# Performance work log

Measured on AMD Instinct MI355X. Metric: run time of the kernel, lower is better.

Reference implementation:

```python
import jax, jax.numpy as jnp
import numpy as np
from jax import lax

# --- static config (mirrors cfg / init args) ---
B, T, F_IN = 4, 1024, 80      # batch, time steps, mel bins (80 -> freq collapses to 1)
C_EMB = 512                   # cfg.dim_embed
C0 = C_EMB // 2               # first_conv_filters (non-tcn branch)
HEADS, K = 8, 7               # num_heads, NA kernel_size (dilation=1)
D_HEAD = C_EMB // HEADS
MLP = 4 * C_EMB               # mlp_ratio=4
EPS = 1e-5                    # layer_norm_eps


def setup_inputs() -> dict:
    key = jax.random.key(0)
    ks = jax.random.split(key, 16)
    rn = lambda k, s, sc=0.02: jax.random.normal(k, s, dtype=jnp.float32) * sc
    z = lambda *s: jnp.zeros(s, dtype=jnp.float32)
    o = lambda *s: jnp.ones(s, dtype=jnp.float32)
    return {
        "x": jax.random.normal(ks[0], (B, 1, T, F_IN), dtype=jnp.float32),
        # conv embedding stack (OIHW)
        "conv0_w": rn(ks[1], (C0, 1, 3, 3), 0.1), "conv0_b": z(C0),
        "conv1_w": rn(ks[2], (C_EMB, C0, 1, 12), 0.02), "conv1_b": z(C_EMB),
        "conv2_w": rn(ks[3], (C_EMB, C_EMB, 3, 3), 0.02), "conv2_b": z(C_EMB),
        "emb_ln_g": o(C_EMB), "emb_ln_b": z(C_EMB),
        # neighborhood attention (linear weights stored [in,out]; apply as x @ W + b)
        "q_w": rn(ks[4], (C_EMB, C_EMB)), "q_b": z(C_EMB),
        "k_w": rn(ks[5], (C_EMB, C_EMB)), "k_b": z(C_EMB),
        "v_w": rn(ks[6], (C_EMB, C_EMB)), "v_b": z(C_EMB),
        "rpb": rn(ks[7], (HEADS, 2 * K - 1)),
        "attn_out_w": rn(ks[8], (C_EMB, C_EMB)), "attn_out_b": z(C_EMB),
        "ln1_g": o(C_EMB), "ln1_b": z(C_EMB),
        "ln2_g": o(C_EMB), "ln2_b": z(C_EMB),
        "mlp1_w": rn(ks[9], (C_EMB, MLP)), "mlp1_b": z(MLP),
        "mlp2_w": rn(ks[10], (MLP, C_EMB)), "mlp2_b": z(C_EMB),
    }


def _layer_norm(x, g, b):
    m = jnp.mean(x, axis=-1, keepdims=True)
    v = jnp.mean(jnp.square(x - m), axis=-1, keepdims=True)
    return (x - m) * lax.rsqrt(v + EPS) * g + b


def _na1d(q, k, v, rpb):
    """1D neighborhood attention (natten1dqkrpb + softmax + natten1dav), dilation=1.
    q,k,v: [B,H,T,D]; rpb: [H,2K-1]. Returns [B,H,T,D]."""
    Bq, H, Tq, D = q.shape
    ni = jnp.clip(jnp.arange(Tq) - K // 2, 0, Tq - K)        # window start per query
    idx = ni[:, None] + jnp.arange(K)                         # [T,K] key positions
    k_win = k[:, :, idx]                                      # [B,H,T,K,D]
    v_win = v[:, :, idx]                                      # [B,H,T,K,D]
    scores = jnp.einsum('bhtd,bhtkd->bhtk', q, k_win)
    rel = idx - jnp.arange(Tq)[:, None] + (K - 1)             # [T,K] in [0,2K-2]
    scores = scores + rpb[:, rel][None]                       # + [1,H,T,K]
    probs = jax.nn.softmax(scores, axis=-1)
    return jnp.einsum('bhtk,bhtkd->bhtd', probs, v_win)


def _forward(x, conv0_w, conv0_b, conv1_w, conv1_b, conv2_w, conv2_b,
             emb_ln_g, emb_ln_b, q_w, q_b, k_w, k_b, v_w, v_b, rpb,
             attn_out_w, attn_out_b, ln1_g, ln1_b, ln2_g, ln2_b,
             mlp1_w, mlp1_b, mlp2_w, mlp2_b):
    conv = lambda h, w, b, pad: lax.conv_general_dilated(
        h, w, (1, 1), pad, dimension_numbers=('NCHW', 'OIHW', 'NCHW')
    ) + b[None, :, None, None]
    pool3 = lambda h: lax.reduce_window(h, -jnp.inf, lax.max,
                                        (1, 1, 1, 3), (1, 1, 1, 3), 'VALID')
    # --- AllInOneEmbeddings (eval: dropouts are no-ops) ---
    h = jax.nn.relu(pool3(conv(x, conv0_w, conv0_b, [(1, 1), (0, 0)])))
    h = jax.nn.relu(pool3(conv(h, conv1_w, conv1_b, [(0, 0), (0, 0)])))
    h = jax.nn.relu(pool3(conv(h, conv2_w, conv2_b, [(1, 1), (0, 0)])))
    h = jnp.transpose(h[..., 0], (0, 2, 1))                   # [B,T,C]
    emb = _layer_norm(h, emb_ln_g, emb_ln_b)
    # --- DinatLayer1d (double_attention=False, drop_path=0) ---
    Bh, Th, Ch = emb.shape
    shortcut = emb
    hs = _layer_norm(emb, ln1_g, ln1_b)
    heads = lambda y: jnp.transpose(y.reshape(Bh, Th, HEADS, D_HEAD), (0, 2, 1, 3))
    q = heads(hs @ q_w + q_b) * (1.0 / jnp.sqrt(jnp.float32(D_HEAD)))
    kk = heads(hs @ k_w + k_b)
    vv = heads(hs @ v_w + v_b)
    ctx = _na1d(q, kk, vv, rpb)                               # [B,H,T,D]
    ctx = jnp.transpose(ctx, (0, 2, 1, 3)).reshape(Bh, Th, Ch)
    attn = ctx @ attn_out_w + attn_out_b                      # NeighborhoodAttentionOutput
    hs = shortcut + attn
    ln = _layer_norm(hs, ln2_g, ln2_b)
    mlp = jax.nn.gelu(ln @ mlp1_w + mlp1_b, approximate=False) @ mlp2_w + mlp2_b
    return hs + mlp


def reference(x, conv0_w, conv0_b, conv1_w, conv1_b, conv2_w, conv2_b,
              emb_ln_g, emb_ln_b, q_w, q_b, k_w, k_b, v_w, v_b, rpb,
              attn_out_w, attn_out_b, ln1_g, ln1_b, ln2_g, ln2_b,
              mlp1_w, mlp1_b, mlp2_w, mlp2_b):
    return _forward(x, conv0_w, conv0_b, conv1_w, conv1_b, conv2_w, conv2_b,
                    emb_ln_g, emb_ln_b, q_w, q_b, k_w, k_b, v_w, v_b, rpb,
                    attn_out_w, attn_out_b, ln1_g, ln1_b, ln2_g, ln2_b,
                    mlp1_w, mlp1_b, mlp2_w, mlp2_b)
```

## Files before the change

kernel.cpp:

```cpp
#include <hip/hip_runtime.h>
#include <hip/hip_bf16.h>
#include <math.h>


typedef __bf16 bf16x8 __attribute__((ext_vector_type(8)));
typedef float f32x4 __attribute__((ext_vector_type(4)));

static __device__ __forceinline__ short f2bf(float f) {
  __hip_bfloat16 h = __float2bfloat16(f);
  return __builtin_bit_cast(short, h);
}

static __device__ __forceinline__ float wave_sum(float v) {
#pragma unroll
  for (int o = 32; o; o >>= 1) v += __shfl_xor(v, o);
  return v;
}

static __device__ __forceinline__ void gld16(const void* g, void* l) {
  __builtin_amdgcn_global_load_lds(
      (const __attribute__((address_space(1))) unsigned int*)g,
      (__attribute__((address_space(3))) unsigned int*)l, 16, 0, 0);
}

__global__ __launch_bounds__(256) void conv0_kernel(
    const float* __restrict__ x, const float* __restrict__ w,
    const float* __restrict__ bias, short* __restrict__ h0) {
  const int b = blockIdx.x >> 10;
  const int t = blockIdx.x & 1023;
  const int c = threadIdx.x;
  __shared__ float xs[3][80];
  for (int i = threadIdx.x; i < 240; i += 256) {
    int dt = i / 80, f = i - dt * 80;
    int tt = t + dt - 1;
    xs[dt][f] = (tt >= 0 && tt < 1024) ? x[(b * 1024 + tt) * 80 + f] : 0.f;
  }
  float wr[9];
#pragma unroll
  for (int i = 0; i < 9; ++i) wr[i] = w[c * 9 + i];
  const float bi = bias[c];
  __syncthreads();
  const int cc = c >> 5, q = (c >> 3) & 3, e = c & 7;
  short* outb = &h0[((size_t)(b * 8 + cc) * 1024 + t) * 896];
  for (int fo = 0; fo < 26; ++fo) {
    float m = -1e30f;
#pragma unroll
    for (int p = 0; p < 3; ++p) {
      const int f = fo * 3 + p;
      float acc = bi;
#pragma unroll
      for (int dt = 0; dt < 3; ++dt)
#pragma unroll
        for (int df = 0; df < 3; ++df)
          acc += xs[dt][f + df] * wr[dt * 3 + df];
      m = fmaxf(m, acc);
    }
    const int row = t * 28 + fo;
    outb[fo * 32 + (q ^ ((row >> 1) & 3)) * 8 + e] = f2bf(fmaxf(m, 0.f));
  }
  if (c < 64) outb[832 + c] = 0;
}

__global__ __launch_bounds__(256) void prep_w1(const float* __restrict__ w,
                                               short* __restrict__ wt) {
  const int co = blockIdx.x;
  __shared__ float ls[3072];
  for (int i = threadIdx.x; i < 3072; i += 256) ls[i] = w[co * 3072 + i];
  __syncthreads();
  const int swz = (co >> 1) & 3;
  for (int i = threadIdx.x; i < 3072; i += 256) {
    const int e = i & 7, q = (i >> 3) & 3, kw = (i >> 5) % 12, cc = i / 384;
    const int ci = cc * 32 + q * 8 + e;
    wt[(((size_t)(cc * 12 + kw) * 512 + co) * 4 + (q ^ swz)) * 8 + e] =
        f2bf(ls[ci * 12 + kw]);
  }
}

__global__ __launch_bounds__(256) void prep_w2(const float* __restrict__ w,
                                               short* __restrict__ wt) {
  const int co = blockIdx.x;
  __shared__ float ls[4608];
  for (int i = threadIdx.x; i < 4608; i += 256) ls[i] = w[co * 4608 + i];
  __syncthreads();
  const int swz = (co >> 1) & 3;
  for (int i = threadIdx.x; i < 4608; i += 256) {
    const int e = i & 7, q = (i >> 3) & 3, p = (i >> 5) % 9, cc = i / 288;
    const int ci = cc * 32 + q * 8 + e;
    wt[(((size_t)(cc * 9 + p) * 512 + co) * 4 + (q ^ swz)) * 8 + e] =
        f2bf(ls[ci * 9 + p]);
  }
}

__global__ void prep_wt(const float* __restrict__ w, short* __restrict__ wt,
                        int K, int N) {
  __shared__ float tile[32][33];
  const int k0 = blockIdx.x * 32, n0 = blockIdx.y * 32;
  const int tx = threadIdx.x, ty = threadIdx.y;
  for (int r = ty; r < 32; r += 8) tile[r][tx] = w[(size_t)(k0 + r) * N + n0 + tx];
  __syncthreads();
  for (int r = ty; r < 32; r += 8) wt[(size_t)(n0 + r) * K + k0 + tx] = f2bf(tile[tx][r]);
}

__global__ __launch_bounds__(256) void zero_h1_edges(short* __restrict__ h1) {
  short* base = h1 + (size_t)blockIdx.x * 164160;
  for (int i = threadIdx.x; i < 160; i += 256) {
    base[i] = 0;
    base[1025 * 160 + i] = 0;
  }
}

__global__ __launch_bounds__(512) void conv1_kernel(
    const short* __restrict__ h0, const short* __restrict__ wt1,
    const float* __restrict__ bias, short* __restrict__ h1) {
  const int b = blockIdx.x >> 5;
  const int t0 = (blockIdx.x & 31) * 32;
  const int co0 = blockIdx.y * 128;
  __shared__ short XsF[2][28672];
  __shared__ short AsF[2][8192];
  const int tid = threadIdx.x;
  const int lane = tid & 63;
  const int wid = tid >> 6;
  const int wm = wid >> 2;
  const int wn = wid & 3;
  const int l15 = lane & 15, lg = lane >> 4;

  const f32x4 zf = {0.f, 0.f, 0.f, 0.f};
  f32x4 acc[4][8];
#pragma unroll
  for (int i = 0; i < 4; ++i)
#pragma unroll
    for (int j = 0; j < 8; ++j) acc[i][j] = zf;

  auto stageX = [&](int cc, int buf) {
    const short* xs = h0 + ((size_t)(b * 8 + cc) * 1024 + t0) * 896;
#pragma unroll
    for (int i = 0; i < 7; ++i) {
      const int v = wid * 7 + i;
      gld16(xs + v * 512 + lane * 8, &XsF[buf][v * 512]);
    }
  };
  auto stageA = [&](int cc, int g, int buf) {
#pragma unroll
    for (int i = 0; i < 2; ++i) {
      const int u = wid * 2 + i;
      const int kwl = u >> 3, r = u & 7;
      gld16(wt1 + ((size_t)((cc * 12 + g * 2 + kwl) * 512) + co0) * 32 +
                r * 512 + lane * 8,
            &AsF[buf][kwl * 4096 + r * 512]);
    }
  };

  stageX(0, 0);
  stageA(0, 0, 0);
  asm volatile("s_waitcnt vmcnt(0)" ::: "memory");
  __builtin_amdgcn_s_barrier();

  for (int s = 0; s < 48; ++s) {
    const int cc = s / 6, g = s - cc * 6;
    if (s < 47) {
      const int s1 = s + 1;
      const int cc1 = s1 / 6, g1 = s1 - cc1 * 6;
      stageA(cc1, g1, s1 & 1);
      if (g1 == 0) {
        stageX(cc1, cc1 & 1);
        asm volatile("s_waitcnt vmcnt(9)" ::: "memory");
      } else {
        asm volatile("s_waitcnt vmcnt(2)" ::: "memory");
      }
    } else {
      asm volatile("s_waitcnt vmcnt(0)" ::: "memory");
    }
    __builtin_amdgcn_s_barrier();
    const short* Xb = XsF[cc & 1];
    const short* Ab = AsF[s & 1];
#pragma unroll
    for (int j = 0; j < 2; ++j) {
      const int kw = g * 2 + j;
      bf16x8 a[4];
#pragma unroll
      for (int sm = 0; sm < 4; ++sm) {
        const int co_l = wm * 64 + sm * 16 + l15;
        a[sm] = *reinterpret_cast<const bf16x8*>(
            &Ab[(j * 512 + co_l * 4 + (lg ^ ((co_l >> 1) & 3))) * 8]);
      }
#pragma unroll
      for (int sn = 0; sn < 8; ++sn) {
        const int row = (wn * 8 + sn) * 28 + l15 + kw;
        bf16x8 bf = *reinterpret_cast<const bf16x8*>(
            &Xb[(row * 4 + (lg ^ ((row >> 1) & 3))) * 8]);
#pragma unroll
        for (int sm = 0; sm < 4; ++sm)
          acc[sm][sn] = __builtin_amdgcn_mfma_f32_16x16x32_bf16(a[sm], bf, acc[sm][sn], 0, 0, 0);
      }
    }
    asm volatile("" ::: "memory");
    __builtin_amdgcn_s_barrier();
  }
  const int basel = lane & 48;
  const int wsrc = (l15 < 5) ? 3 * l15 : 0;
#pragma unroll
  for (int sm = 0; sm < 4; ++sm)
#pragma unroll
    for (int sn = 0; sn < 8; ++sn) {
      const int t = t0 + wn * 8 + sn;
#pragma unroll
      for (int r = 0; r < 4; ++r) {
        float val = acc[sm][sn][r];
        float v0 = __shfl(val, basel + wsrc);
        float v1 = __shfl(val, basel + wsrc + 1);
        float v2 = __shfl(val, basel + wsrc + 2);
        if (l15 < 5) {
          const int co = co0 + wm * 64 + sm * 16 + lg * 4 + r;
          float p = fmaxf(fmaxf(v0, v1), v2) + bias[co];
          const int cc2 = co >> 5, q = (co >> 3) & 3, e = co & 7;
          const int row_g = (t + 1) * 5 + l15;
          h1[((size_t)(b * 16 + cc2) * 1026 + (t + 1)) * 160 + l15 * 32 +
             (q ^ ((row_g >> 1) & 3)) * 8 + e] = f2bf(fmaxf(p, 0.f));
        }
      }
    }
}

__global__ __launch_bounds__(512) void conv2_kernel(
    const short* __restrict__ h1, const short* __restrict__ wt2,
    const float* __restrict__ bias, float* __restrict__ emb_in) {
  const int b = blockIdx.x >> 5;
  const int t0 = (blockIdx.x & 31) * 32;
  const int co0 = blockIdx.y * 128;
  __shared__ __align__(16) short smem2[35840];
  const int tid = threadIdx.x;
  const int lane = tid & 63;
  const int wid = tid >> 6;
  const int wm = wid >> 1;
  const int wn = wid & 1;
  const int l15 = lane & 15, lg = lane >> 4;
  const f32x4 zf = {0.f, 0.f, 0.f, 0.f};
  f32x4 acc[2][3];
#pragma unroll
  for (int i = 0; i < 2; ++i)
#pragma unroll
    for (int j = 0; j < 3; ++j) acc[i][j] = zf;
  int tl[3], dwl[3];
#pragma unroll
  for (int sn = 0; sn < 3; ++sn) {
    const int c = wn * 48 + sn * 16 + l15;
    tl[sn] = c / 3;
    dwl[sn] = c - tl[sn] * 3;
  }

  auto stageX = [&](int cc, int buf) {
    const short* xs = h1 + ((size_t)(b * 16 + cc) * 1026 + t0) * 160;
#pragma unroll
    for (int i = 0; i < 2; ++i) {
      const int v = wid + 8 * i;
      if (v < 11) gld16(xs + v * 512 + lane * 8, &smem2[buf * 5632 + v * 512]);
    }
  };
  auto stageA = [&](int cc, int g, int buf) {
#pragma unroll
    for (int i = 0; i < 3; ++i) {
      const int u = wid * 3 + i;
      const int pl = u >> 3, r = u & 7;
      gld16(wt2 + ((size_t)((cc * 9 + g * 3 + pl) * 512) + co0) * 32 +
                r * 512 + lane * 8,
            &smem2[11264 + buf * 12288 + pl * 4096 + r * 512]);
    }
  };

  stageX(0, 0);
  stageA(0, 0, 0);
  asm volatile("s_waitcnt vmcnt(0)" ::: "memory");
  __builtin_amdgcn_s_barrier();

  for (int s = 0; s < 48; ++s) {
    const int cc = s / 3, g = s - cc * 3;
    if (s < 47) {
      const int s1 = s + 1;
      const int cc1 = s1 / 3, g1 = s1 - cc1 * 3;
      stageA(cc1, g1, s1 & 1);
      if (g1 == 0) {
        stageX(cc1, cc1 & 1);
        if (wid < 3) asm volatile("s_waitcnt vmcnt(5)" ::: "memory");
        else         asm volatile("s_waitcnt vmcnt(4)" ::: "memory");
      } else {
        asm volatile("s_waitcnt vmcnt(3)" ::: "memory");
      }
    } else {
      asm volatile("s_waitcnt vmcnt(0)" ::: "memory");
    }
    __builtin_amdgcn_s_barrier();
    const short* Xb = &smem2[(cc & 1) * 5632];
    const short* Ab = &smem2[11264 + (s & 1) * 12288];
#pragma unroll
    for (int j = 0; j < 3; ++j) {
      bf16x8 a[2];
#pragma unroll
      for (int sm = 0; sm < 2; ++sm) {
        const int co_l = wm * 32 + sm * 16 + l15;
        a[sm] = *reinterpret_cast<const bf16x8*>(
            &Ab[(j * 512 + co_l * 4 + (lg ^ ((co_l >> 1) & 3))) * 8]);
      }
#pragma unroll
      for (int sn = 0; sn < 3; ++sn) {
        const int row = (tl[sn] + g) * 5 + dwl[sn] + j;
        bf16x8 xv = *reinterpret_cast<const bf16x8*>(
            &Xb[(row * 4 + (lg ^ ((row >> 1) & 3))) * 8]);
#pragma unroll
        for (int sm = 0; sm < 2; ++sm)
          acc[sm][sn] = __builtin_amdgcn_mfma_f32_16x16x32_bf16(a[sm], xv, acc[sm][sn], 0, 0, 0);
      }
    }
    asm volatile("" ::: "memory");
    __builtin_amdgcn_s_barrier();
  }
  float(*Ds)[100] = reinterpret_cast<float(*)[100]>(smem2);
#pragma unroll
  for (int sm = 0; sm < 2; ++sm)
#pragma unroll
    for (int sn = 0; sn < 3; ++sn)
#pragma unroll
      for (int r = 0; r < 4; ++r)
        Ds[wm * 32 + sm * 16 + lg * 4 + r][wn * 48 + sn * 16 + l15] = acc[sm][sn][r];
  __syncthreads();
  for (int e = tid; e < 4096; e += 512) {
    const int co = e & 127, tt = e >> 7;
    float m = fmaxf(fmaxf(Ds[co][tt * 3], Ds[co][tt * 3 + 1]), Ds[co][tt * 3 + 2]) + bias[co0 + co];
    emb_in[((size_t)(b * 1024) + t0 + tt) * 512 + co0 + co] = fmaxf(m, 0.f);
  }
}

__global__ __launch_bounds__(256) void ln_double_kernel(
    const float* __restrict__ x, const float* __restrict__ g0,
    const float* __restrict__ b0, const float* __restrict__ g1,
    const float* __restrict__ b1, float* __restrict__ o0, float* __restrict__ o1) {
  const int row = blockIdx.x * 4 + (threadIdx.x >> 6);
  const int lane = threadIdx.x & 63;
  const float* xr = x + (size_t)row * 512;
  float v[8];
#pragma unroll
  for (int j = 0; j < 8; ++j) v[j] = xr[j * 64 + lane];
  float s = 0;
#pragma unroll
  for (int j = 0; j < 8; ++j) s += v[j];
  s = wave_sum(s);
  const float mean = s * (1.f / 512.f);
  float q = 0;
#pragma unroll
  for (int j = 0; j < 8; ++j) { float d = v[j] - mean; q += d * d; }
  q = wave_sum(q);
  const float rs = rsqrtf(q * (1.f / 512.f) + 1e-5f);
#pragma unroll
  for (int j = 0; j < 8; ++j) {
    const int ci = j * 64 + lane;
    float e = (v[j] - mean) * rs * g0[ci] + b0[ci];
    o0[(size_t)row * 512 + ci] = e;
    v[j] = e;
  }
  s = 0;
#pragma unroll
  for (int j = 0; j < 8; ++j) s += v[j];
  s = wave_sum(s);
  const float mean2 = s * (1.f / 512.f);
  q = 0;
#pragma unroll
  for (int j = 0; j < 8; ++j) { float d = v[j] - mean2; q += d * d; }
  q = wave_sum(q);
  const float rs2 = rsqrtf(q * (1.f / 512.f) + 1e-5f);
#pragma unroll
  for (int j = 0; j < 8; ++j) {
    const int ci = j * 64 + lane;
    o1[(size_t)row * 512 + ci] = (v[j] - mean2) * rs2 * g1[ci] + b1[ci];
  }
}

__global__ __launch_bounds__(256) void ln_kernel(
    const float* __restrict__ x, const float* __restrict__ g,
    const float* __restrict__ b, float* __restrict__ o) {
  const int row = blockIdx.x * 4 + (threadIdx.x >> 6);
  const int lane = threadIdx.x & 63;
  const float* xr = x + (size_t)row * 512;
  float v[8];
#pragma unroll
  for (int j = 0; j < 8; ++j) v[j] = xr[j * 64 + lane];
  float s = 0;
#pragma unroll
  for (int j = 0; j < 8; ++j) s += v[j];
  s = wave_sum(s);
  const float mean = s * (1.f / 512.f);
  float q = 0;
#pragma unroll
  for (int j = 0; j < 8; ++j) { float d = v[j] - mean; q += d * d; }
  q = wave_sum(q);
  const float rs = rsqrtf(q * (1.f / 512.f) + 1e-5f);
#pragma unroll
  for (int j = 0; j < 8; ++j) {
    const int ci = j * 64 + lane;
    o[(size_t)row * 512 + ci] = (v[j] - mean) * rs * g[ci] + b[ci];
  }
}

__global__ __launch_bounds__(256) void na1d_kernel(
    const float* __restrict__ q, const float* __restrict__ k,
    const float* __restrict__ v, const float* __restrict__ rpb,
    float* __restrict__ ctx) {
  const int W = blockIdx.x * 4 + (threadIdx.x >> 6);
  const int lane = threadIdx.x & 63;
  const int b = W >> 13, h = (W >> 10) & 7, t = W & 1023;
  int ni = t - 3;
  ni = ni < 0 ? 0 : (ni > 1017 ? 1017 : ni);
  const size_t base = (size_t)(b * 1024) * 512 + h * 64;
  const float qv = q[base + (size_t)t * 512 + lane];
  const float* kb = k + base + (size_t)ni * 512;
  float s[7];
#pragma unroll
  for (int j = 0; j < 7; ++j) {
    float pd = qv * kb[j * 512 + lane];
    pd = wave_sum(pd);
    s[j] = pd + rpb[h * 13 + (ni + j - t + 6)];
  }
  float mx = s[0];
#pragma unroll
  for (int j = 1; j < 7; ++j) mx = fmaxf(mx, s[j]);
  float den = 0;
#pragma unroll
  for (int j = 0; j < 7; ++j) { s[j] = expf(s[j] - mx); den += s[j]; }
  const float inv = 1.f / den;
  const float* vb = v + base + (size_t)ni * 512;
  float o = 0;
#pragma unroll
  for (int j = 0; j < 7; ++j) o += s[j] * vb[j * 512 + lane];
  ctx[base + (size_t)t * 512 + lane] = o * inv;
}

template <int EPI>
__global__ __launch_bounds__(256) void gemm_tf(
    const float* __restrict__ A, const short* __restrict__ Wt,
    const float* __restrict__ bias, const float* __restrict__ res,
    float* __restrict__ C, int K, int N) {
  const int m0 = blockIdx.x * 128, n0 = blockIdx.y * 64;
  __shared__ short Asm[128][40];
  __shared__ short Bsm[64][40];
  const int tid = threadIdx.x;
  const int wid = tid >> 6, lane = tid & 63;
  const int wm = wid >> 1, wn = wid & 1;
  const int l15 = lane & 15, lg = lane >> 4;
  const f32x4 zf = {0.f, 0.f, 0.f, 0.f};
  f32x4 acc[4][2];
#pragma unroll
  for (int i = 0; i < 4; ++i) { acc[i][0] = zf; acc[i][1] = zf; }
  const int ar = tid >> 1, ahf = (tid & 1) * 16;
  for (int k0 = 0; k0 < K; k0 += 32) {
    __syncthreads();
    {
      const float4* s = reinterpret_cast<const float4*>(&A[(size_t)(m0 + ar) * K + k0 + ahf]);
      float4 f0 = s[0], f1 = s[1], f2 = s[2], f3 = s[3];
      short* d = &Asm[ar][ahf];
      d[0] = f2bf(f0.x);  d[1] = f2bf(f0.y);  d[2] = f2bf(f0.z);  d[3] = f2bf(f0.w);
      d[4] = f2bf(f1.x);  d[5] = f2bf(f1.y);  d[6] = f2bf(f1.z);  d[7] = f2bf(f1.w);
      d[8] = f2bf(f2.x);  d[9] = f2bf(f2.y);  d[10] = f2bf(f2.z); d[11] = f2bf(f2.w);
      d[12] = f2bf(f3.x); d[13] = f2bf(f3.y); d[14] = f2bf(f3.z); d[15] = f2bf(f3.w);
    }
    if (tid < 128) {
      const int br = tid >> 1, bhf = (tid & 1) * 16;
      const int4* s = reinterpret_cast<const int4*>(&Wt[(size_t)(n0 + br) * K + k0 + bhf]);
      int4* d = reinterpret_cast<int4*>(&Bsm[br][bhf]);
      d[0] = s[0];
      d[1] = s[1];
    }
    __syncthreads();
    bf16x8 bfr[2];
#pragma unroll
    for (int sn = 0; sn < 2; ++sn)
      bfr[sn] = *reinterpret_cast<const bf16x8*>(&Bsm[wn * 32 + sn * 16 + l15][lg * 8]);
#pragma unroll
    for (int sm = 0; sm < 4; ++sm) {
      bf16x8 a = *reinterpret_cast<const bf16x8*>(&Asm[wm * 64 + sm * 16 + l15][lg * 8]);
#pragma unroll
      for (int sn = 0; sn < 2; ++sn)
        acc[sm][sn] = __builtin_amdgcn_mfma_f32_16x16x32_bf16(a, bfr[sn], acc[sm][sn], 0, 0, 0);
    }
  }
#pragma unroll
  for (int sm = 0; sm < 4; ++sm)
#pragma unroll
    for (int sn = 0; sn < 2; ++sn)
#pragma unroll
      for (int r = 0; r < 4; ++r) {
        const int m = m0 + wm * 64 + sm * 16 + lg * 4 + r;
        const int n = n0 + wn * 32 + sn * 16 + l15;
        float val = acc[sm][sn][r] + bias[n];
        if (EPI == 1) val *= 0.125f;
        if (EPI == 2) val = 0.5f * val * (1.f + erff(val * 0.70710678f));
        if (EPI == 3) val += res[(size_t)m * N + n];
        C[(size_t)m * N + n] = val;
      }
}

extern "C" void kernel_launch(void* const* d_in, const int* in_sizes, int n_in,
                              void* d_out, int out_size, void* d_ws, size_t ws_size,
                              hipStream_t stream) {
  (void)in_sizes; (void)n_in; (void)out_size;
  const float* x        = (const float*)d_in[0];
  const float* conv0_w  = (const float*)d_in[1];
  const float* conv0_b  = (const float*)d_in[2];
  const float* conv1_w  = (const float*)d_in[3];
  const float* conv1_b  = (const float*)d_in[4];
  const float* conv2_w  = (const float*)d_in[5];
  const float* conv2_b  = (const float*)d_in[6];
  const float* emb_ln_g = (const float*)d_in[7];
  const float* emb_ln_b = (const float*)d_in[8];
  const float* q_w  = (const float*)d_in[9];
  const float* q_b  = (const float*)d_in[10];
  const float* k_w  = (const float*)d_in[11];
  const float* k_b  = (const float*)d_in[12];
  const float* v_w  = (const float*)d_in[13];
  const float* v_b  = (const float*)d_in[14];
  const float* rpb  = (const float*)d_in[15];
  const float* ao_w = (const float*)d_in[16];
  const float* ao_b = (const float*)d_in[17];
  const float* ln1_g = (const float*)d_in[18];
  const float* ln1_b = (const float*)d_in[19];
  const float* ln2_g = (const float*)d_in[20];
  const float* ln2_b = (const float*)d_in[21];
  const float* m1_w = (const float*)d_in[22];
  const float* m1_b = (const float*)d_in[23];
  const float* m2_w = (const float*)d_in[24];
  const float* m2_b = (const float*)d_in[25];

  char* ws = (char*)d_ws;
  size_t off = 0;
  auto alloc = [&](size_t bytes) -> char* {
    char* p = ws + off;
    off += (bytes + 255) & ~(size_t)255;
    return p;
  };
  short* h0   = (short*)alloc(4ull * 8 * 1024 * 896 * 2);
  short* h1   = (short*)alloc(4ull * 16 * 1026 * 160 * 2);
  float* embi = (float*)alloc(4ull * 1024 * 512 * 4);
  float* emb  = (float*)alloc(4ull * 1024 * 512 * 4);
  float* hs1  = (float*)alloc(4ull * 1024 * 512 * 4);
  float* qb   = (float*)alloc(4ull * 1024 * 512 * 4);
  float* kb   = (float*)alloc(4ull * 1024 * 512 * 4);
  float* vb   = (float*)alloc(4ull * 1024 * 512 * 4);
  float* ctx  = (float*)alloc(4ull * 1024 * 512 * 4);
  float* hs   = (float*)alloc(4ull * 1024 * 512 * 4);
  short* wt1  = (short*)alloc(512ull * 12 * 256 * 2);
  short* wt2  = (short*)alloc(512ull * 9 * 512 * 2);
  short* wtq  = (short*)alloc(512ull * 512 * 2);
  short* wtk  = (short*)alloc(512ull * 512 * 2);
  short* wtv  = (short*)alloc(512ull * 512 * 2);
  short* wtao = (short*)alloc(512ull * 512 * 2);
  short* wtm1 = (short*)alloc(2048ull * 512 * 2);
  short* wtm2 = (short*)alloc(512ull * 2048 * 2);
  if (ws_size < off) return;
  float* mid  = (float*)h0;
  float* ln2o = embi;
  float* outp = (float*)d_out;

  prep_w1<<<512, 256, 0, stream>>>(conv1_w, wt1);
  prep_w2<<<512, 256, 0, stream>>>(conv2_w, wt2);
  zero_h1_edges<<<64, 256, 0, stream>>>(h1);
  dim3 tb(32, 8);
  prep_wt<<<dim3(16, 16), tb, 0, stream>>>(q_w, wtq, 512, 512);
  prep_wt<<<dim3(16, 16), tb, 0, stream>>>(k_w, wtk, 512, 512);
  prep_wt<<<dim3(16, 16), tb, 0, stream>>>(v_w, wtv, 512, 512);
  prep_wt<<<dim3(16, 16), tb, 0, stream>>>(ao_w, wtao, 512, 512);
  prep_wt<<<dim3(16, 64), tb, 0, stream>>>(m1_w, wtm1, 512, 2048);
  prep_wt<<<dim3(64, 16), tb, 0, stream>>>(m2_w, wtm2, 2048, 512);

  conv0_kernel<<<4096, 256, 0, stream>>>(x, conv0_w, conv0_b, h0);
  conv1_kernel<<<dim3(128, 4), 512, 0, stream>>>(h0, wt1, conv1_b, h1);
  conv2_kernel<<<dim3(128, 4), 512, 0, stream>>>(h1, wt2, conv2_b, embi);
  ln_double_kernel<<<1024, 256, 0, stream>>>(embi, emb_ln_g, emb_ln_b, ln1_g, ln1_b, emb, hs1);
  gemm_tf<1><<<dim3(32, 8), 256, 0, stream>>>(hs1, wtq, q_b, nullptr, qb, 512, 512);
  gemm_tf<0><<<dim3(32, 8), 256, 0, stream>>>(hs1, wtk, k_b, nullptr, kb, 512, 512);
  gemm_tf<0><<<dim3(32, 8), 256, 0, stream>>>(hs1, wtv, v_b, nullptr, vb, 512, 512);
  na1d_kernel<<<8192, 256, 0, stream>>>(qb, kb, vb, rpb, ctx);
  gemm_tf<3><<<dim3(32, 8), 256, 0, stream>>>(ctx, wtao, ao_b, emb, hs, 512, 512);
  ln_kernel<<<1024, 256, 0, stream>>>(hs, ln2_g, ln2_b, ln2o);
  gemm_tf<2><<<dim3(32, 32), 256, 0, stream>>>(ln2o, wtm1, m1_b, nullptr, mid, 512, 2048);
  gemm_tf<3><<<dim3(32, 8), 256, 0, stream>>>(mid, wtm2, m2_b, hs, outp, 2048, 512);
}
```

Measured before the change: 499.5 us.

## Fuse Q/K/V projections into one GEMM and retile conv1 with 32x32 MFMA

Concatenates the Q, K and V weights and biases so a single GEMM over N=1536 writes an interleaved qkv buffer, and the neighborhood-attention kernel reads from it with stride 1536. This replaces three launches with one larger grid. Separately, conv1 is restructured to 256-thread blocks over 16 time steps, at two blocks per CU, using 32x32x16 MFMA fragments. Its input X tile is now single-buffered while the weight tiles keep a two-stage ring, which may expose load latency at channel-chunk boundaries.

New measurement: 526.0 us. 1.05x slower.

```diff
diff --git a/kernel.cpp b/kernel.cpp
--- a/kernel.cpp
+++ b/kernel.cpp
@@ -5,6 +5,7 @@
 
 typedef __bf16 bf16x8 __attribute__((ext_vector_type(8)));
 typedef float f32x4 __attribute__((ext_vector_type(4)));
+typedef float f32x16 __attribute__((ext_vector_type(16)));
 
 static __device__ __forceinline__ short f2bf(float f) {
   __hip_bfloat16 h = __float2bfloat16(f);
@@ -109,108 +110,121 @@
   }
 }
 
-__global__ __launch_bounds__(512) void conv1_kernel(
+__global__ __launch_bounds__(256) void concat3_kernel(
+    const float* __restrict__ a, const float* __restrict__ b,
+    const float* __restrict__ c, float* __restrict__ o) {
+  const int i = blockIdx.x * 256 + threadIdx.x;
+  o[i] = i < 512 ? a[i] : (i < 1024 ? b[i - 512] : c[i - 1024]);
+}
+
+__global__ __launch_bounds__(256, 2) void conv1_kernel(
     const short* __restrict__ h0, const short* __restrict__ wt1,
     const float* __restrict__ bias, short* __restrict__ h1) {
-  const int b = blockIdx.x >> 5;
-  const int t0 = (blockIdx.x & 31) * 32;
+  const int b = blockIdx.x >> 6;
+  const int t0 = (blockIdx.x & 63) * 16;
   const int co0 = blockIdx.y * 128;
-  __shared__ short XsF[2][28672];
-  __shared__ short AsF[2][8192];
+  __shared__ short Xs[14336];
+  __shared__ short As[2][8192];
   const int tid = threadIdx.x;
   const int lane = tid & 63;
   const int wid = tid >> 6;
-  const int wm = wid >> 2;
-  const int wn = wid & 3;
-  const int l15 = lane & 15, lg = lane >> 4;
-
-  const f32x4 zf = {0.f, 0.f, 0.f, 0.f};
-  f32x4 acc[4][8];
-#pragma unroll
-  for (int i = 0; i < 4; ++i)
-#pragma unroll
-    for (int j = 0; j < 8; ++j) acc[i][j] = zf;
-
-  auto stageX = [&](int cc, int buf) {
+  const int wm = wid >> 1, wn = wid & 1;
+  const int l31 = lane & 31, lh = lane >> 5, l15 = lane & 15;
+
+  f32x16 acc[2][4];
+#pragma unroll
+  for (int i = 0; i < 2; ++i)
+#pragma unroll
+    for (int j = 0; j < 4; ++j)
+#pragma unroll
+      for (int r = 0; r < 16; ++r) acc[i][j][r] = 0.f;
+
+  auto stageX = [&](int cc) {
     const short* xs = h0 + ((size_t)(b * 8 + cc) * 1024 + t0) * 896;
 #pragma unroll
     for (int i = 0; i < 7; ++i) {
       const int v = wid * 7 + i;
-      gld16(xs + v * 512 + lane * 8, &XsF[buf][v * 512]);
+      gld16(xs + v * 512 + lane * 8, &Xs[v * 512]);
     }
   };
   auto stageA = [&](int cc, int g, int buf) {
 #pragma unroll
-    for (int i = 0; i < 2; ++i) {
-      const int u = wid * 2 + i;
+    for (int i = 0; i < 4; ++i) {
+      const int u = wid * 4 + i;
       const int kwl = u >> 3, r = u & 7;
       gld16(wt1 + ((size_t)((cc * 12 + g * 2 + kwl) * 512) + co0) * 32 +
                 r * 512 + lane * 8,
-            &AsF[buf][kwl * 4096 + r * 512]);
+            &As[buf][kwl * 4096 + r * 512]);
     }
   };
 
-  stageX(0, 0);
+  stageX(0);
   stageA(0, 0, 0);
-  asm volatile("s_waitcnt vmcnt(0)" ::: "memory");
+  stageA(0, 1, 1);
+  asm volatile("s_waitcnt vmcnt(4)" ::: "memory");
   __builtin_amdgcn_s_barrier();
 
-  for (int s = 0; s < 48; ++s) {
-    const int cc = s / 6, g = s - cc * 6;
-    if (s < 47) {
-      const int s1 = s + 1;
-      const int cc1 = s1 / 6, g1 = s1 - cc1 * 6;
-      stageA(cc1, g1, s1 & 1);
-      if (g1 == 0) {
-        stageX(cc1, cc1 & 1);
-        asm volatile("s_waitcnt vmcnt(9)" ::: "memory");
-      } else {
-        asm volatile("s_waitcnt vmcnt(2)" ::: "memory");
-      }
-    } else {
-      asm volatile("s_waitcnt vmcnt(0)" ::: "memory");
-    }
-    __builtin_amdgcn_s_barrier();
-    const short* Xb = XsF[cc & 1];
-    const short* Ab = AsF[s & 1];
-#pragma unroll
-    for (int j = 0; j < 2; ++j) {
-      const int kw = g * 2 + j;
-      bf16x8 a[4];
-#pragma unroll
-      for (int sm = 0; sm < 4; ++sm) {
-        const int co_l = wm * 64 + sm * 16 + l15;
-        a[sm] = *reinterpret_cast<const bf16x8*>(
-            &Ab[(j * 512 + co_l * 4 + (lg ^ ((co_l >> 1) & 3))) * 8]);
-      }
-#pragma unroll
-      for (int sn = 0; sn < 8; ++sn) {
-        const int row = (wn * 8 + sn) * 28 + l15 + kw;
-        bf16x8 bf = *reinterpret_cast<const bf16x8*>(
-            &Xb[(row * 4 + (lg ^ ((row >> 1) & 3))) * 8]);
-#pragma unroll
-        for (int sm = 0; sm < 4; ++sm)
-          acc[sm][sn] = __builtin_amdgcn_mfma_f32_16x16x32_bf16(a[sm], bf, acc[sm][sn], 0, 0, 0);
-      }
-    }
-    asm volatile("" ::: "memory");
-    __builtin_amdgcn_s_barrier();
-  }
+  for (int cc = 0; cc < 8; ++cc) {
+    for (int g = 0; g < 6; ++g) {
+      const short* Ab = As[g & 1];
+#pragma unroll
+      for (int j = 0; j < 2; ++j) {
+        const int kw = g * 2 + j;
+#pragma unroll
+        for (int ks = 0; ks < 2; ++ks) {
+          const int q = ks * 2 + lh;
+          bf16x8 a[2];
+#pragma unroll
+          for (int fm = 0; fm < 2; ++fm) {
+            const int co_l = wm * 64 + fm * 32 + l31;
+            a[fm] = *reinterpret_cast<const bf16x8*>(
+                &Ab[j * 4096 + (co_l * 4 + (q ^ ((co_l >> 1) & 3))) * 8]);
+          }
+#pragma unroll
+          for (int fn = 0; fn < 4; ++fn) {
+            const int col = wn * 128 + fn * 32 + l31;
+            const int row = (col >> 4) * 28 + (col & 15) + kw;
+            bf16x8 bx = *reinterpret_cast<const bf16x8*>(
+                &Xs[(row * 4 + (q ^ ((row >> 1) & 3))) * 8]);
+#pragma unroll
+            for (int fm = 0; fm < 2; ++fm)
+              acc[fm][fn] = __builtin_amdgcn_mfma_f32_32x32x16_bf16(
+                  a[fm], bx, acc[fm][fn], 0, 0, 0);
+          }
+        }
+      }
+      asm volatile("" ::: "memory");
+      __builtin_amdgcn_s_barrier();
+      if (g < 4) {
+        stageA(cc, g + 2, g & 1);
+        asm volatile("s_waitcnt vmcnt(4)" ::: "memory");
+      } else if (g == 4) {
+        asm volatile("s_waitcnt vmcnt(0)" ::: "memory");
+      } else if (cc < 7) {
+        stageX(cc + 1);
+        stageA(cc + 1, 0, 0);
+        stageA(cc + 1, 1, 1);
+        asm volatile("s_waitcnt vmcnt(4)" ::: "memory");
+      }
+      __builtin_amdgcn_s_barrier();
+    }
+  }
+
   const int basel = lane & 48;
   const int wsrc = (l15 < 5) ? 3 * l15 : 0;
 #pragma unroll
-  for (int sm = 0; sm < 4; ++sm)
-#pragma unroll
-    for (int sn = 0; sn < 8; ++sn) {
-      const int t = t0 + wn * 8 + sn;
-#pragma unroll
-      for (int r = 0; r < 4; ++r) {
-        float val = acc[sm][sn][r];
+  for (int fm = 0; fm < 2; ++fm)
+#pragma unroll
+    for (int fn = 0; fn < 4; ++fn) {
+      const int t = t0 + wn * 8 + fn * 2 + ((lane >> 4) & 1);
+#pragma unroll
+      for (int r = 0; r < 16; ++r) {
+        float val = acc[fm][fn][r];
         float v0 = __shfl(val, basel + wsrc);
         float v1 = __shfl(val, basel + wsrc + 1);
         float v2 = __shfl(val, basel + wsrc + 2);
         if (l15 < 5) {
-          const int co = co0 + wm * 64 + sm * 16 + lg * 4 + r;
+          const int co = co0 + wm * 64 + fm * 32 + (r & 3) + 8 * (r >> 2) + 4 * lh;
           float p = fmaxf(fmaxf(v0, v1), v2) + bias[co];
           const int cc2 = co >> 5, q = (co >> 3) & 3, e = co & 7;
           const int row_g = (t + 1) * 5 + l15;
@@ -400,21 +414,19 @@
 }
 
 __global__ __launch_bounds__(256) void na1d_kernel(
-    const float* __restrict__ q, const float* __restrict__ k,
-    const float* __restrict__ v, const float* __restrict__ rpb,
+    const float* __restrict__ qkv, const float* __restrict__ rpb,
     float* __restrict__ ctx) {
   const int W = blockIdx.x * 4 + (threadIdx.x >> 6);
   const int lane = threadIdx.x & 63;
   const int b = W >> 13, h = (W >> 10) & 7, t = W & 1023;
   int ni = t - 3;
   ni = ni < 0 ? 0 : (ni > 1017 ? 1017 : ni);
-  const size_t base = (size_t)(b * 1024) * 512 + h * 64;
-  const float qv = q[base + (size_t)t * 512 + lane];
-  const float* kb = k + base + (size_t)ni * 512;
+  const float qv = qkv[((size_t)(b * 1024) + t) * 1536 + h * 64 + lane];
+  const float* kb = qkv + 512 + ((size_t)(b * 1024) + ni) * 1536 + h * 64;
   float s[7];
 #pragma unroll
   for (int j = 0; j < 7; ++j) {
-    float pd = qv * kb[j * 512 + lane];
+    float pd = qv * kb[j * 1536 + lane];
     pd = wave_sum(pd);
     s[j] = pd + rpb[h * 13 + (ni + j - t + 6)];
   }
@@ -425,11 +437,11 @@
 #pragma unroll
   for (int j = 0; j < 7; ++j) { s[j] = expf(s[j] - mx); den += s[j]; }
   const float inv = 1.f / den;
-  const float* vb = v + base + (size_t)ni * 512;
+  const float* vb = qkv + 1024 + ((size_t)(b * 1024) + ni) * 1536 + h * 64;
   float o = 0;
 #pragma unroll
-  for (int j = 0; j < 7; ++j) o += s[j] * vb[j * 512 + lane];
-  ctx[base + (size_t)t * 512 + lane] = o * inv;
+  for (int j = 0; j < 7; ++j) o += s[j] * vb[j * 1536 + lane];
+  ctx[((size_t)(b * 1024) + t) * 512 + h * 64 + lane] = o * inv;
 }
 
 template <int EPI>
@@ -489,9 +501,9 @@
         const int m = m0 + wm * 64 + sm * 16 + lg * 4 + r;
         const int n = n0 + wn * 32 + sn * 16 + l15;
         float val = acc[sm][sn][r] + bias[n];
-        if (EPI == 1) val *= 0.125f;
         if (EPI == 2) val = 0.5f * val * (1.f + erff(val * 0.70710678f));
         if (EPI == 3) val += res[(size_t)m * N + n];
+        if (EPI == 4 && n < 512) val *= 0.125f;
         C[(size_t)m * N + n] = val;
       }
 }
@@ -539,19 +551,16 @@
   float* embi = (float*)alloc(4ull * 1024 * 512 * 4);
   float* emb  = (float*)alloc(4ull * 1024 * 512 * 4);
   float* hs1  = (float*)alloc(4ull * 1024 * 512 * 4);
-  float* qb   = (float*)alloc(4ull * 1024 * 512 * 4);
-  float* kb   = (float*)alloc(4ull * 1024 * 512 * 4);
-  float* vb   = (float*)alloc(4ull * 1024 * 512 * 4);
+  float* qkv  = (float*)alloc(4ull * 1024 * 1536 * 4);
   float* ctx  = (float*)alloc(4ull * 1024 * 512 * 4);
   float* hs   = (float*)alloc(4ull * 1024 * 512 * 4);
   short* wt1  = (short*)alloc(512ull * 12 * 256 * 2);
   short* wt2  = (short*)alloc(512ull * 9 * 512 * 2);
-  short* wtq  = (short*)alloc(512ull * 512 * 2);
-  short* wtk  = (short*)alloc(512ull * 512 * 2);
-  short* wtv  = (short*)alloc(512ull * 512 * 2);
+  short* wtqkv = (short*)alloc(1536ull * 512 * 2);
   short* wtao = (short*)alloc(512ull * 512 * 2);
   short* wtm1 = (short*)alloc(2048ull * 512 * 2);
   short* wtm2 = (short*)alloc(512ull * 2048 * 2);
+  float* qkvb = (float*)alloc(1536ull * 4);
   if (ws_size < off) return;
   float* mid  = (float*)h0;
   float* ln2o = embi;
@@ -560,22 +569,21 @@
   prep_w1<<<512, 256, 0, stream>>>(conv1_w, wt1);
   prep_w2<<<512, 256, 0, stream>>>(conv2_w, wt2);
   zero_h1_edges<<<64, 256, 0, stream>>>(h1);
+  concat3_kernel<<<6, 256, 0, stream>>>(q_b, k_b, v_b, qkvb);
   dim3 tb(32, 8);
-  prep_wt<<<dim3(16, 16), tb, 0, stream>>>(q_w, wtq, 512, 512);
-  prep_wt<<<dim3(16, 16), tb, 0, stream>>>(k_w, wtk, 512, 512);
-  prep_wt<<<dim3(16, 16), tb, 0, stream>>>(v_w, wtv, 512, 512);
+  prep_wt<<<dim3(16, 16), tb, 0, stream>>>(q_w, wtqkv, 512, 512);
+  prep_wt<<<dim3(16, 16), tb, 0, stream>>>(k_w, wtqkv + 512 * 512, 512, 512);
+  prep_wt<<<dim3(16, 16), tb, 0, stream>>>(v_w, wtqkv + 1024 * 512, 512, 512);
   prep_wt<<<dim3(16, 16), tb, 0, stream>>>(ao_w, wtao, 512, 512);
   prep_wt<<<dim3(16, 64), tb, 0, stream>>>(m1_w, wtm1, 512, 2048);
   prep_wt<<<dim3(64, 16), tb, 0, stream>>>(m2_w, wtm2, 2048, 512);
 
   conv0_kernel<<<4096, 256, 0, stream>>>(x, conv0_w, conv0_b, h0);
-  conv1_kernel<<<dim3(128, 4), 512, 0, stream>>>(h0, wt1, conv1_b, h1);
+  conv1_kernel<<<dim3(256, 4), 256, 0, stream>>>(h0, wt1, conv1_b, h1);
   conv2_kernel<<<dim3(128, 4), 512, 0, stream>>>(h1, wt2, conv2_b, embi);
   ln_double_kernel<<<1024, 256, 0, stream>>>(embi, emb_ln_g, emb_ln_b, ln1_g, ln1_b, emb, hs1);
-  gemm_tf<1><<<dim3(32, 8), 256, 0, stream>>>(hs1, wtq, q_b, nullptr, qb, 512, 512);
-  gemm_tf<0><<<dim3(32, 8), 256, 0, stream>>>(hs1, wtk, k_b, nullptr, kb, 512, 512);
-  gemm_tf<0><<<dim3(32, 8), 256, 0, stream>>>(hs1, wtv, v_b, nullptr, vb, 512, 512);
-  na1d_kernel<<<8192, 256, 0, stream>>>(qb, kb, vb, rpb, ctx);
+  gemm_tf<4><<<dim3(32, 24), 256, 0, stream>>>(hs1, wtqkv, qkvb, nullptr, qkv, 512, 1536);
+  na1d_kernel<<<8192, 256, 0, stream>>>(qkv, rpb, ctx);
   gemm_tf<3><<<dim3(32, 8), 256, 0, stream>>>(ctx, wtao, ao_b, emb, hs, 512, 512);
   ln_kernel<<<1024, 256, 0, stream>>>(hs, ln2_g, ln2_b, ln2o);
   gemm_tf<2><<<dim3(32, 32), 256, 0, stream>>>(ln2o, wtm1, m1_b, nullptr, mid, 512, 2048);
```
